# Kernel optimization log

Measured on AMD Instinct MI355X. Metric: run time of the kernel, lower is better.

The kernel has to match this reference:

```python
import jax, jax.numpy as jnp
import numpy as np
from jax import lax

G, BS = 8, 32  # group_num, blocksize


def conv(x, w, b=None, stride=1, pad=0):
    out = lax.conv_general_dilated(x, w, (stride, stride), [(pad, pad), (pad, pad)],
                                   dimension_numbers=('NCHW', 'OIHW', 'NCHW'))
    if b is not None:
        out = out + b[None, :, None, None]
    return out


def prelu(x, a):
    return jnp.where(x >= 0, x, a * x)


def reshape_adap(x, bs):
    # faithful vectorized form of My_Reshape_Adap: channel c = co*bs*bs + p*bs + q
    # goes to output[b, co, i*bs+p, j*bs+q]
    B, C, h, w = x.shape
    co = C // (bs * bs)
    return x.reshape(B, co, bs, bs, h, w).transpose(0, 1, 4, 2, 5, 3).reshape(B, co, h * bs, w * bs)


def setup_inputs() -> dict:
    key = jax.random.key(0)
    ks = jax.random.split(key, 24)
    rn = lambda k, shp, s: (jax.random.normal(k, shp, dtype=jnp.float32) * s)
    inp = {
        'x': rn(ks[0], (1, 1, 256, 256), 1.0),
        'sample_w': rn(ks[1], (G, 13, 1, 32, 32), 0.03),
        'up_w': rn(ks[2], (G, 1024, 13, 1, 1), 0.2),
        'up_b': rn(ks[3], (G, 1024), 0.02),
        'h1_w': rn(ks[4], (G, 64, 1, 3, 3), 0.2),
        'h1_b': rn(ks[5], (G, 64), 0.02),
        'h1_a': jnp.full((G,), 0.25, jnp.float32),
        'fus_w': rn(ks[6], (G - 1, 64, 128, 3, 3), 0.03),
        'fus_b': rn(ks[7], (G - 1, 64), 0.02),
        'fus_a': jnp.full((G - 1,), 0.25, jnp.float32),
        't2_w': rn(ks[8], (G, 64, 64, 3, 3), 0.04),
        't2_b': rn(ks[9], (G, 64), 0.02),
        't2_a': jnp.full((G,), 0.25, jnp.float32),
        't3_w': rn(ks[10], (G, 64, 64, 3, 3), 0.04),
        't3_b': rn(ks[11], (G, 64), 0.02),
        't3_a': jnp.full((G,), 0.25, jnp.float32),
        't4_w': rn(ks[12], (G, 64, 64, 3, 3), 0.04),
        't4_b': rn(ks[13], (G, 64), 0.02),
        't4_a': jnp.full((G,), 0.25, jnp.float32),
        't5_w': rn(ks[14], (G, 1, 64, 3, 3), 0.04),
        't5_b': rn(ks[15], (G, 1), 0.02),
    }
    return inp


def reference(x, sample_w, up_w, up_b, h1_w, h1_b, h1_a, fus_w, fus_b, fus_a,
              t2_w, t2_b, t2_a, t3_w, t3_b, t3_a, t4_w, t4_b, t4_a, t5_w, t5_b):
    outs = []
    feature = None
    for m in range(G):
        # SamplingModule: conv(1->13, k=32, s=32, no bias)
        s = conv(x, sample_w[m], stride=BS)
        # HeadBlock: 1x1 upsample (13->1024) + block scatter reshape + conv(1->64)+PReLU
        u = conv(s, up_w[m], up_b[m])
        r = reshape_adap(u, BS)                       # [B,1,H,W]
        h = prelu(conv(r, h1_w[m], h1_b[m], pad=1), h1_a[m])  # [B,64,H,W]
        if m == 0:
            feature = h
        else:
            # Fusion_concate: conv(128->64)+PReLU on channel concat
            cat = jnp.concatenate([feature, h], axis=1)
            feature = prelu(conv(cat, fus_w[m - 1], fus_b[m - 1], pad=1), fus_a[m - 1])
        t = prelu(conv(feature, t2_w[m], t2_b[m], pad=1), t2_a[m])
        t = prelu(conv(t, t3_w[m], t3_b[m], pad=1), t3_a[m])
        t = prelu(conv(t, t4_w[m], t4_b[m], pad=1), t4_a[m])
        outs.append(conv(t, t5_w[m], t5_b[m], pad=1))
    return jnp.stack(outs)  # [G, B, 1, H, W]
```

## Files before the change

### kernel.cpp

```cpp
#include <hip/hip_runtime.h>

constexpr int H = 256, W = 256, NPIX = H * W;
constexpr int PW = 258;
constexpr size_t PLANE = (size_t)PW * PW * 64;

typedef _Float16 half8 __attribute__((ext_vector_type(8)));
typedef _Float16 half4 __attribute__((ext_vector_type(4)));
typedef float    f32x4 __attribute__((ext_vector_type(4)));
typedef float    f32x16 __attribute__((ext_vector_type(16)));

__device__ __forceinline__ void gl16(const _Float16* g, _Float16* l)
{
    __builtin_amdgcn_global_load_lds(
        (const __attribute__((address_space(1))) unsigned int*)g,
        (__attribute__((address_space(3))) unsigned int*)l, 16, 0, 0);
}

__global__ __launch_bounds__(256)
void prep_k(const float* __restrict__ x, const float* __restrict__ sw,
            const float* __restrict__ uw, const float* __restrict__ ub,
            const float* __restrict__ t2w, const float* __restrict__ t3w,
            const float* __restrict__ t4w, const float* __restrict__ fusw,
            _Float16* __restrict__ planes, _Float16* __restrict__ w16,
            float* __restrict__ r_all)
{
    const int b = blockIdx.x, t = threadIdx.x;
    for (int idx = b * 256 + t; idx < 24 * 1028 * 8; idx += 512 * 256) {
        int c = idx & 7, rem = idx >> 3;
        int p = rem / 1028, bb = rem % 1028;
        int gy, gx;
        if (bb < 258)      { gy = 0;            gx = bb; }
        else if (bb < 516) { gy = 257;          gx = bb - 258; }
        else if (bb < 772) { gy = bb - 516 + 1; gx = 0; }
        else               { gy = bb - 772 + 1; gx = 257; }
        f32x4 z = {0.f, 0.f, 0.f, 0.f};
        *(f32x4*)(planes + (size_t)p * PLANE + ((size_t)(gy * PW + gx) * 64) + c * 8) = z;
    }
    for (int idx = b * 256 + t; idx < 38 * 36864; idx += 512 * 256) {
        int blk = idx / 36864, r2 = idx % 36864;
        int e = r2 & 7, co = (r2 >> 3) & 63, hh = (r2 >> 9) & 1, kk = (r2 >> 10) & 3,
            tap = r2 >> 12;
        const float* src; int cin, cib;
        if (blk < 24) {
            int which = blk >> 3, m = blk & 7;
            src = (which == 0 ? t2w : which == 1 ? t3w : t4w) + (size_t)m * 64 * 64 * 9;
            cin = 64; cib = 0;
        } else {
            int f = (blk - 24) >> 1; cib = ((blk - 24) & 1) * 64;
            src = fusw + (size_t)f * 64 * 128 * 9; cin = 128;
        }
        int ci = cib + (kk * 2 + hh) * 8 + e;
        w16[idx] = (_Float16)src[((size_t)co * cin + ci) * 9 + tap];
    }
    {
        int m = b >> 6, ij = b & 63;
        int i = ij >> 3, j = ij & 7;
        __shared__ float s_lds[16];
        if (t < 208) {
            int c = t >> 4, sub = t & 15;
            float acc = 0.f;
            for (int k = sub * 64; k < sub * 64 + 64; ++k) {
                int p = k >> 5, q = k & 31;
                acc += x[(i * 32 + p) * W + (j * 32 + q)] * sw[(m * 13 + c) * 1024 + k];
            }
            #pragma unroll
            for (int off = 8; off; off >>= 1) acc += __shfl_down(acc, off, 16);
            if (sub == 0) s_lds[c] = acc;
        }
        __syncthreads();
        const float* uwm = uw + m * 1024 * 13;
        float* rm = r_all + m * NPIX;
        #pragma unroll
        for (int pi = 0; pi < 4; ++pi) {
            int px = pi * 256 + t;
            int p = px >> 5, q = px & 31;
            int oc = p * 32 + q;
            float acc = ub[m * 1024 + oc];
            #pragma unroll
            for (int c = 0; c < 13; ++c) acc = fmaf(uwm[oc * 13 + c], s_lds[c], acc);
            rm[((i * 32 + p) << 8) + j * 32 + q] = acc;
        }
    }
}

__global__ __launch_bounds__(256)
void h1_k(const float* __restrict__ r_all, const float* __restrict__ w,
          const float* __restrict__ b, const float* __restrict__ a,
          _Float16* __restrict__ f0)
{
    const float* r = r_all;
    const int t = threadIdx.x;
    const int px = t & 63, cog = t >> 6;
    const int y = blockIdx.x >> 2;
    const int x = ((blockIdx.x & 3) << 6) + px;
    float v[9];
    #pragma unroll
    for (int dy = 0; dy < 3; ++dy) {
        int gy = y + dy - 1;
        #pragma unroll
        for (int dx = 0; dx < 3; ++dx) {
            int gx = x + dx - 1;
            v[dy*3+dx] = ((unsigned)gy < 256u && (unsigned)gx < 256u)
                       ? r[(gy << 8) + gx] : 0.f;
        }
    }
    const float slope = a[0];
    _Float16* op = f0 + ((size_t)((y + 1) * PW + (x + 1))) * 64 + cog * 16;
    #pragma unroll
    for (int cg2 = 0; cg2 < 2; ++cg2) {
        half8 o;
        #pragma unroll
        for (int j = 0; j < 8; ++j) {
            int co = cog * 16 + cg2 * 8 + j;
            float acc = b[co];
            #pragma unroll
            for (int k = 0; k < 9; ++k) acc = fmaf(v[k], w[co*9+k], acc);
            acc = acc >= 0.f ? acc : slope * acc;
            o[j] = (_Float16)acc;
        }
        *(half8*)(op + cg2 * 8) = o;
    }
}

__global__ __launch_bounds__(128, 2)
void conv_mfma_k(const _Float16* __restrict__ in0, const _Float16* __restrict__ w0,
                 const float* __restrict__ bias, const float* __restrict__ alpha,
                 _Float16* __restrict__ out)
{
    const int t    = threadIdx.x;
    const int lane = t & 63;
    const int wv   = t >> 6;
    const int b    = blockIdx.x;
    const int m    = b >> 7;
    const int rem  = b & 127;
    const int xq   = rem & 3;
    const int y0   = (rem >> 2) << 3;
    const int x0   = xq << 6;

    const _Float16* inp0 = in0 + (size_t)m * PLANE;
    _Float16*       outp = out + (size_t)m * PLANE;
    const _Float16* wp0  = w0 + (size_t)m * 36864;
    const float*    bp   = bias + m * 64;
    const float     slope = alpha[m];

    const int h = lane >> 5, cl = lane & 31;
    const int cobase = wv * 32;

    extern __shared__ __align__(16) char smem[];
    _Float16* li = (_Float16*)smem;

    half8 Areg[36];
    #pragma unroll
    for (int tap = 0; tap < 9; ++tap)
        #pragma unroll
        for (int kk = 0; kk < 4; ++kk)
            Areg[tap*4+kk] = *(const half8*)(wp0 +
                (size_t)(((tap*4+kk)*2 + h)*64 + cobase + cl) * 8);

    auto stage_row = [&](int pr) {
        const int slot = pr & 3;
        #pragma unroll
        for (int i = 0; i < 5; ++i) {
            int f = i * 128 + t;
            if (i < 4 || f < 528) {
                int hx = f >> 3, c = f & 7;
                gl16(inp0 + ((size_t)(pr * PW + x0 + hx) * 64 + (c ^ (hx & 7)) * 8),
                     li + (size_t)(slot * 528 + f) * 8);
            }
        }
    };

    f32x16 acc0, acc1;

    stage_row(y0); stage_row(y0 + 1); stage_row(y0 + 2);
    __syncthreads();
    #pragma unroll 1
    for (int s = 0; s < 8; ++s) {
        if (s < 7) stage_row(y0 + s + 3);
        #pragma unroll
        for (int q = 0; q < 4; ++q)
            #pragma unroll
            for (int j = 0; j < 4; ++j) {
                float bb = bp[cobase + q * 8 + 4 * h + j];
                acc0[q*4+j] = bb; acc1[q*4+j] = bb;
            }
        __builtin_amdgcn_s_setprio(1);
        #pragma unroll
        for (int tap = 0; tap < 9; ++tap) {
            const int dy = tap / 3, dx = tap % 3;
            const int slot = (y0 + s + dy) & 3;
            const int hx0 = cl + dx;
            const int hx1 = hx0 + 32;
            const int sw8 = hx0 & 7;
            #pragma unroll
            for (int kk = 0; kk < 4; ++kk) {
                const int c = kk * 2 + h;
                half8 b0 = *(const half8*)(li + ((size_t)(slot*528 + hx0*8 + (c ^ sw8))) * 8);
                half8 b1 = *(const half8*)(li + ((size_t)(slot*528 + hx1*8 + (c ^ sw8))) * 8);
                acc0 = __builtin_amdgcn_mfma_f32_32x32x16_f16(Areg[tap*4+kk], b0, acc0, 0, 0, 0);
                acc1 = __builtin_amdgcn_mfma_f32_32x32x16_f16(Areg[tap*4+kk], b1, acc1, 0, 0, 0);
            }
        }
        __builtin_amdgcn_s_setprio(0);
        const int y = y0 + s;
        #pragma unroll
        for (int pt = 0; pt < 2; ++pt) {
            const size_t gp = (size_t)((y + 1) * PW + (x0 + pt * 32 + cl + 1)) * 64;
            const f32x16& A0 = pt ? acc1 : acc0;
            #pragma unroll
            for (int q = 0; q < 4; ++q) {
                half4 v0;
                #pragma unroll
                for (int j = 0; j < 4; ++j) {
                    float xv = A0[q*4+j];
                    xv = xv >= 0.f ? xv : slope * xv;
                    v0[j] = (_Float16)v0[j];
                    v0[j] = (_Float16)xv;
                }
                *(half4*)(outp + gp + cobase + q * 8 + 4 * h) = v0;
            }
        }
        if (s < 7) {
            asm volatile("s_waitcnt vmcnt(8)" ::: "memory");
            __builtin_amdgcn_s_barrier();
            __builtin_amdgcn_sched_barrier(0);
        }
    }
}

__global__ __launch_bounds__(256, 2)
void fus_k(const _Float16* __restrict__ fprev, const float* __restrict__ rm,
           const float* __restrict__ h1w, const float* __restrict__ h1b,
           const float* __restrict__ h1a,
           const _Float16* __restrict__ wf, const _Float16* __restrict__ wh,
           const float* __restrict__ bias, const float* __restrict__ alpha,
           _Float16* __restrict__ outp)
{
    const int t = threadIdx.x, lane = t & 63, wv = t >> 6;
    const int b = blockIdx.x;
    const int xcd = b & 7, u = b >> 3, xq = u & 3, band = u >> 2;
    const int y0 = xcd * 32 + band * 2, x0 = xq * 64;
    const int h = lane >> 5, cl = lane & 31;
    const int px0 = (wv & 1) * 32, cobase = (wv >> 1) * 32;

    __shared__ __align__(16) _Float16 ringF[4 * 528 * 8];
    __shared__ __align__(16) _Float16 ringH[4 * 528 * 8];

    #pragma unroll
    for (int i = 0; i < 9; ++i) {
        int idx = i * 256 + t;
        if (i < 8 || idx < 2112) {
            int r = idx / 528, f = idx - r * 528;
            int hx = f >> 3, c = f & 7;
            gl16(fprev + ((size_t)((y0 + r) * PW + x0 + hx) * 64 + (c ^ (hx & 7)) * 8),
                 ringF + (size_t)idx * 8);
        }
    }
    {
        const int c8 = t & 7;
        float wreg[72];
        #pragma unroll
        for (int i = 0; i < 18; ++i)
            *(f32x4*)(wreg + i * 4) = *(const f32x4*)(h1w + c8 * 72 + i * 4);
        float b8[8];
        #pragma unroll
        for (int j = 0; j < 8; ++j) b8[j] = h1b[c8 * 8 + j];
        const float hs = h1a[0];

        #pragma unroll
        for (int it = 0; it < 9; ++it) {
            int idx = it * 256 + t;
            if (it < 8 || idx < 2112) {
                int pl = idx >> 3;
                int r  = pl / 66, hx = pl - r * 66;
                int gy = y0 - 1 + r, gx = x0 - 1 + hx;
                half8 o = {0,0,0,0,0,0,0,0};
                if ((unsigned)gy < 256u && (unsigned)gx < 256u) {
                    float v[9];
                    #pragma unroll
                    for (int dy = 0; dy < 3; ++dy) {
                        int ry = gy + dy - 1;
                        #pragma unroll
                        for (int dx = 0; dx < 3; ++dx) {
                            int rx = gx + dx - 1;
                            v[dy*3+dx] = ((unsigned)ry < 256u && (unsigned)rx < 256u)
                                       ? rm[(ry << 8) + rx] : 0.f;
                        }
                    }
                    #pragma unroll
                    for (int j = 0; j < 8; ++j) {
                        float av = b8[j];
                        #pragma unroll
                        for (int k = 0; k < 9; ++k) av = fmaf(v[k], wreg[j*9+k], av);
                        av = av >= 0.f ? av : hs * av;
                        o[j] = (_Float16)av;
                    }
                }
                *(half8*)(ringH + (size_t)(r * 528 + hx * 8 + (c8 ^ (hx & 7))) * 8) = o;
            }
        }
    }
    __builtin_amdgcn_sched_barrier(0);

    half8 Areg[36];
    auto load_A = [&](const _Float16* w) {
        #pragma unroll
        for (int tap = 0; tap < 9; ++tap)
            #pragma unroll
            for (int kk = 0; kk < 4; ++kk)
                Areg[tap*4+kk] = *(const half8*)(w +
                    (size_t)(((tap*4+kk)*2 + h)*64 + cobase + cl) * 8);
    };
    load_A(wf);

    f32x16 acc0, acc1;
    #pragma unroll
    for (int q = 0; q < 4; ++q)
        #pragma unroll
        for (int j = 0; j < 4; ++j) {
            float bb = bias[cobase + q * 8 + 4 * h + j];
            acc0[q*4+j] = bb; acc1[q*4+j] = bb;
        }

    __syncthreads();

    auto cpass = [&](const _Float16* ring) {
        __builtin_amdgcn_s_setprio(1);
        #pragma unroll
        for (int tap = 0; tap < 9; ++tap) {
            const int dy = tap / 3, dx = tap % 3;
            const int hx = px0 + cl + dx;
            const int sw = hx & 7;
            #pragma unroll
            for (int kk = 0; kk < 4; ++kk) {
                const int c = kk * 2 + h;
                half8 b0 = *(const half8*)(ring + ((size_t)(((dy    )*528) + hx*8 + (c ^ sw))) * 8);
                half8 b1 = *(const half8*)(ring + ((size_t)(((dy + 1)*528) + hx*8 + (c ^ sw))) * 8);
                acc0 = __builtin_amdgcn_mfma_f32_32x32x16_f16(Areg[tap*4+kk], b0, acc0, 0, 0, 0);
                acc1 = __builtin_amdgcn_mfma_f32_32x32x16_f16(Areg[tap*4+kk], b1, acc1, 0, 0, 0);
            }
        }
        __builtin_amdgcn_s_setprio(0);
    };

    cpass(ringF);
    load_A(wh);
    cpass(ringH);

    const float slope = alpha[0];
    #pragma unroll
    for (int s = 0; s < 2; ++s) {
        const size_t gp = (size_t)((y0 + s + 1) * PW + (x0 + px0 + cl + 1)) * 64 + cobase;
        const f32x16& A0 = s ? acc1 : acc0;
        #pragma unroll
        for (int q = 0; q < 4; ++q) {
            half4 v;
            #pragma unroll
            for (int j = 0; j < 4; ++j) {
                float xv = A0[q*4+j];
                xv = xv >= 0.f ? xv : slope * xv;
                v[j] = (_Float16)xv;
            }
            *(half4*)(outp + gp + q * 8 + 4 * h) = v;
        }
    }
}

__global__ __launch_bounds__(256, 2)
void t5_k(const _Float16* __restrict__ in_all, const float* __restrict__ w_all,
          const float* __restrict__ b_all, float* __restrict__ out_all)
{
    const int m = blockIdx.y;
    const _Float16* in = in_all + (size_t)m * PLANE;
    const float* w = w_all + m * 576;
    float* outp = out_all + m * NPIX;

    const int t = threadIdx.x;
    const int b = blockIdx.x;
    const int xcd = b & 7, u = b >> 3;
    const int xh = u & 1, band = u >> 1;
    const int y0 = xcd * 32 + band * 8;
    const int x0 = xh << 7;

    __shared__ __align__(16) _Float16 ring[4 * 130 * 64];
    __shared__ float wl[576];
    __shared__ float part[128];

    auto stage_row = [&](int pr) {
        const int slot = pr & 3;
        #pragma unroll
        for (int i = 0; i < 5; ++i) {
            int f = i * 256 + t;
            if (i < 4 || f < 1040) {
                int hx = f >> 3, c = f & 7;
                gl16(in + ((size_t)(pr * PW + x0 + hx) * 64 + (c ^ (hx & 7)) * 8),
                     ring + (size_t)(slot * 1040 + f) * 8);
            }
        }
    };

    stage_row(y0); stage_row(y0 + 1); stage_row(y0 + 2);
    #pragma unroll
    for (int i = 0; i < 3; ++i) { int idx = i*256 + t; if (idx < 576) wl[idx] = w[idx]; }
    __syncthreads();

    const int p = t & 127, chalf = t >> 7;
    #pragma unroll 1
    for (int s = 0; s < 8; ++s) {
        if (s < 7) stage_row(y0 + s + 3);
        float acc = 0.f;
        #pragma unroll
        for (int dy = 0; dy < 3; ++dy) {
            const int slot = (y0 + s + dy) & 3;
            #pragma unroll
            for (int dx = 0; dx < 3; ++dx) {
                const int hx = p + dx, sw = hx & 7, tap = dy * 3 + dx;
                #pragma unroll
                for (int kc = 0; kc < 4; ++kc) {
                    const int c8 = chalf * 4 + kc;
                    half8 vv = *(const half8*)(ring +
                        ((size_t)((slot*130 + hx)*8 + (c8 ^ sw))) * 8);
                    #pragma unroll
                    for (int e = 0; e < 8; ++e)
                        acc = fmaf((float)vv[e], wl[(c8 * 8 + e) * 9 + tap], acc);
                }
            }
        }
        if (chalf) part[p] = acc;
        __syncthreads();
        if (!chalf) outp[((y0 + s) << 8) + x0 + p] = part[p] + acc + b_all[m];
        __syncthreads();
    }
}

extern "C" void kernel_launch(void* const* d_in, const int* in_sizes, int n_in,
                              void* d_out, int out_size, void* d_ws, size_t ws_size,
                              hipStream_t stream)
{
    const float* x        = (const float*)d_in[0];
    const float* sample_w = (const float*)d_in[1];
    const float* up_w     = (const float*)d_in[2];
    const float* up_b     = (const float*)d_in[3];
    const float* h1_w     = (const float*)d_in[4];
    const float* h1_b     = (const float*)d_in[5];
    const float* h1_a     = (const float*)d_in[6];
    const float* fus_w    = (const float*)d_in[7];
    const float* fus_b    = (const float*)d_in[8];
    const float* fus_a    = (const float*)d_in[9];
    const float* t2_w     = (const float*)d_in[10];
    const float* t2_b     = (const float*)d_in[11];
    const float* t2_a     = (const float*)d_in[12];
    const float* t3_w     = (const float*)d_in[13];
    const float* t3_b     = (const float*)d_in[14];
    const float* t3_a     = (const float*)d_in[15];
    const float* t4_w     = (const float*)d_in[16];
    const float* t4_b     = (const float*)d_in[17];
    const float* t4_a     = (const float*)d_in[18];
    const float* t5_w     = (const float*)d_in[19];
    const float* t5_b     = (const float*)d_in[20];

    float* out = (float*)d_out;
    char*  wsb = (char*)d_ws;

    _Float16* w16    = (_Float16*)wsb;
    float*    r_all  = (float*)(wsb + 2801664);
    _Float16* f_all  = (_Float16*)(wsb + 4898816);
    _Float16* sc_all = f_all + 8 * PLANE;
    _Float16* t1_all = sc_all + 8 * PLANE;

    auto wblk = [&](int b) { return w16 + (size_t)b * 36864; };

    prep_k<<<512, 256, 0, stream>>>(x, sample_w, up_w, up_b,
                                    t2_w, t3_w, t4_w, fus_w,
                                    f_all, w16, r_all);
    h1_k<<<1024, 256, 0, stream>>>(r_all, h1_w, h1_b, h1_a, f_all);

    for (int m = 1; m < 8; ++m) {
        fus_k<<<512, 256, 0, stream>>>(
            f_all + (size_t)(m - 1) * PLANE,
            r_all + m * NPIX, h1_w + m * 576, h1_b + m * 64, h1_a + m,
            wblk(24 + (m - 1) * 2), wblk(24 + (m - 1) * 2 + 1),
            fus_b + (m - 1) * 64, fus_a + (m - 1),
            f_all + (size_t)m * PLANE);
    }

    const size_t LDSB = 33792;
    conv_mfma_k<<<1024, 128, LDSB, stream>>>(f_all, wblk(0), t2_b, t2_a, t1_all);
    conv_mfma_k<<<1024, 128, LDSB, stream>>>(t1_all, wblk(8), t3_b, t3_a, sc_all);
    conv_mfma_k<<<1024, 128, LDSB, stream>>>(sc_all, wblk(16), t4_b, t4_a, t1_all);
    t5_k<<<dim3(64, 8), 256, 0, stream>>>(t1_all, t5_w, t5_b, out);
}
```

Before: 393.2 us.

## Retile tail convs so each wave computes all 64 output channels over wider strips

The three 64->64 tail convolutions are re-tiled so each block covers a 128-pixel-wide strip with 8 rows, and each wave computes all 64 output channels for 64 pixels using four MFMA accumulators instead of 32 channels. Each B fragment read from LDS now feeds two MFMAs, which cuts LDS read traffic per MFMA and halves the number of blocks. The cost is twice the weight registers (72 half8) and twice the LDS per block (66560 bytes), with launch bounds dropped to one block per CU-slot. Occupancy falls and register pressure may cause spills.

```diff
diff --git a/kernel.cpp b/kernel.cpp
--- a/kernel.cpp
+++ b/kernel.cpp
@@ -122,7 +122,7 @@
     }
 }
 
-__global__ __launch_bounds__(128, 2)
+__global__ __launch_bounds__(128, 1)
 void conv_mfma_k(const _Float16* __restrict__ in0, const _Float16* __restrict__ w0,
                  const float* __restrict__ bias, const float* __restrict__ alpha,
                  _Float16* __restrict__ out)
@@ -131,11 +131,11 @@
     const int lane = t & 63;
     const int wv   = t >> 6;
     const int b    = blockIdx.x;
-    const int m    = b >> 7;
-    const int rem  = b & 127;
-    const int xq   = rem & 3;
-    const int y0   = (rem >> 2) << 3;
-    const int x0   = xq << 6;
+    const int m    = b >> 6;
+    const int rem  = b & 63;
+    const int xh   = rem & 1;
+    const int y0   = (rem >> 1) << 3;
+    const int x0   = xh << 7;
 
     const _Float16* inp0 = in0 + (size_t)m * PLANE;
     _Float16*       outp = out + (size_t)m * PLANE;
@@ -144,33 +144,36 @@
     const float     slope = alpha[m];
 
     const int h = lane >> 5, cl = lane & 31;
-    const int cobase = wv * 32;
+    const int px0 = wv << 6;
 
     extern __shared__ __align__(16) char smem[];
     _Float16* li = (_Float16*)smem;
 
-    half8 Areg[36];
+    half8 Areg0[36], Areg1[36];
     #pragma unroll
     for (int tap = 0; tap < 9; ++tap)
         #pragma unroll
-        for (int kk = 0; kk < 4; ++kk)
-            Areg[tap*4+kk] = *(const half8*)(wp0 +
-                (size_t)(((tap*4+kk)*2 + h)*64 + cobase + cl) * 8);
+        for (int kk = 0; kk < 4; ++kk) {
+            Areg0[tap*4+kk] = *(const half8*)(wp0 +
+                (size_t)(((tap*4+kk)*2 + h)*64 + cl) * 8);
+            Areg1[tap*4+kk] = *(const half8*)(wp0 +
+                (size_t)(((tap*4+kk)*2 + h)*64 + 32 + cl) * 8);
+        }
 
     auto stage_row = [&](int pr) {
         const int slot = pr & 3;
         #pragma unroll
-        for (int i = 0; i < 5; ++i) {
+        for (int i = 0; i < 9; ++i) {
             int f = i * 128 + t;
-            if (i < 4 || f < 528) {
+            if (i < 8 || f < 1040) {
                 int hx = f >> 3, c = f & 7;
                 gl16(inp0 + ((size_t)(pr * PW + x0 + hx) * 64 + (c ^ (hx & 7)) * 8),
-                     li + (size_t)(slot * 528 + f) * 8);
+                     li + (size_t)(slot * 1040 + f) * 8);
             }
         }
     };
 
-    f32x16 acc0, acc1;
+    f32x16 acc00, acc01, acc10, acc11;
 
     stage_row(y0); stage_row(y0 + 1); stage_row(y0 + 2);
     __syncthreads();
@@ -181,47 +184,51 @@
         for (int q = 0; q < 4; ++q)
             #pragma unroll
             for (int j = 0; j < 4; ++j) {
-                float bb = bp[cobase + q * 8 + 4 * h + j];
-                acc0[q*4+j] = bb; acc1[q*4+j] = bb;
+                float b0 = bp[q * 8 + 4 * h + j];
+                float b1 = bp[32 + q * 8 + 4 * h + j];
+                acc00[q*4+j] = b0; acc01[q*4+j] = b0;
+                acc10[q*4+j] = b1; acc11[q*4+j] = b1;
             }
         __builtin_amdgcn_s_setprio(1);
         #pragma unroll
         for (int tap = 0; tap < 9; ++tap) {
             const int dy = tap / 3, dx = tap % 3;
             const int slot = (y0 + s + dy) & 3;
-            const int hx0 = cl + dx;
+            const int hx0 = px0 + cl + dx;
             const int hx1 = hx0 + 32;
             const int sw8 = hx0 & 7;
             #pragma unroll
             for (int kk = 0; kk < 4; ++kk) {
                 const int c = kk * 2 + h;
-                half8 b0 = *(const half8*)(li + ((size_t)(slot*528 + hx0*8 + (c ^ sw8))) * 8);
-                half8 b1 = *(const half8*)(li + ((size_t)(slot*528 + hx1*8 + (c ^ sw8))) * 8);
-                acc0 = __builtin_amdgcn_mfma_f32_32x32x16_f16(Areg[tap*4+kk], b0, acc0, 0, 0, 0);
-                acc1 = __builtin_amdgcn_mfma_f32_32x32x16_f16(Areg[tap*4+kk], b1, acc1, 0, 0, 0);
+                half8 b0 = *(const half8*)(li + ((size_t)(slot*1040 + hx0*8 + (c ^ sw8))) * 8);
+                half8 b1 = *(const half8*)(li + ((size_t)(slot*1040 + hx1*8 + (c ^ sw8))) * 8);
+                acc00 = __builtin_amdgcn_mfma_f32_32x32x16_f16(Areg0[tap*4+kk], b0, acc00, 0, 0, 0);
+                acc01 = __builtin_amdgcn_mfma_f32_32x32x16_f16(Areg0[tap*4+kk], b1, acc01, 0, 0, 0);
+                acc10 = __builtin_amdgcn_mfma_f32_32x32x16_f16(Areg1[tap*4+kk], b0, acc10, 0, 0, 0);
+                acc11 = __builtin_amdgcn_mfma_f32_32x32x16_f16(Areg1[tap*4+kk], b1, acc11, 0, 0, 0);
             }
         }
         __builtin_amdgcn_s_setprio(0);
         const int y = y0 + s;
         #pragma unroll
         for (int pt = 0; pt < 2; ++pt) {
-            const size_t gp = (size_t)((y + 1) * PW + (x0 + pt * 32 + cl + 1)) * 64;
-            const f32x16& A0 = pt ? acc1 : acc0;
+            const size_t gp = (size_t)((y + 1) * PW + (x0 + px0 + pt * 32 + cl + 1)) * 64;
+            const f32x16& A0 = pt ? acc01 : acc00;
+            const f32x16& A1 = pt ? acc11 : acc10;
             #pragma unroll
             for (int q = 0; q < 4; ++q) {
-                half4 v0;
+                half4 v0, v1;
                 #pragma unroll
                 for (int j = 0; j < 4; ++j) {
-                    float xv = A0[q*4+j];
-                    xv = xv >= 0.f ? xv : slope * xv;
-                    v0[j] = (_Float16)v0[j];
-                    v0[j] = (_Float16)xv;
+                    float xv = A0[q*4+j]; xv = xv >= 0.f ? xv : slope * xv; v0[j] = (_Float16)xv;
+                    float yv = A1[q*4+j]; yv = yv >= 0.f ? yv : slope * yv; v1[j] = (_Float16)yv;
                 }
-                *(half4*)(outp + gp + cobase + q * 8 + 4 * h) = v0;
+                *(half4*)(outp + gp + q * 8 + 4 * h)      = v0;
+                *(half4*)(outp + gp + 32 + q * 8 + 4 * h) = v1;
             }
         }
         if (s < 7) {
-            asm volatile("s_waitcnt vmcnt(8)" ::: "memory");
+            asm volatile("s_waitcnt vmcnt(16)" ::: "memory");
             __builtin_amdgcn_s_barrier();
             __builtin_amdgcn_sched_barrier(0);
         }
@@ -484,9 +491,9 @@
             f_all + (size_t)m * PLANE);
     }
 
-    const size_t LDSB = 33792;
-    conv_mfma_k<<<1024, 128, LDSB, stream>>>(f_all, wblk(0), t2_b, t2_a, t1_all);
-    conv_mfma_k<<<1024, 128, LDSB, stream>>>(t1_all, wblk(8), t3_b, t3_a, sc_all);
-    conv_mfma_k<<<1024, 128, LDSB, stream>>>(sc_all, wblk(16), t4_b, t4_a, t1_all);
+    const size_t LDSB = 66560;
+    conv_mfma_k<<<512, 128, LDSB, stream>>>(f_all, wblk(0), t2_b, t2_a, t1_all);
+    conv_mfma_k<<<512, 128, LDSB, stream>>>(t1_all, wblk(8), t3_b, t3_a, sc_all);
+    conv_mfma_k<<<512, 128, LDSB, stream>>>(sc_all, wblk(16), t4_b, t4_a, t1_all);
     t5_k<<<dim3(64, 8), 256, 0, stream>>>(t1_all, t5_w, t5_b, out);
 }
```

Result: no change. 399.0 us (+1.5%).

## Fuse t4 conv with final t5 conv and widen conv_mfma tiles to 128 pixels

Applied to the files above, without the earlier changes.

Fuses the t4 64->64 MFMA conv with the 64->1 t5 conv. The t4 output rows are kept in an LDS ring and t5 is computed from them directly, with halo columns shared between neighbouring tiles via atomicAdd onto an output that prep_k pre-fills with the t5 bias. This removes one full 64-channel fp16 plane write and read-back per group. Separately, conv_mfma_k now uses 256 threads covering 128 pixels per block, doubling LDS to 66560 bytes, so each staged row is shared across more pixels. The costs are one recomputed halo row above and below each band, atomics at tile edges, and possibly lower occupancy from the larger LDS footprint.

```diff
diff --git a/kernel.cpp b/kernel.cpp
--- a/kernel.cpp
+++ b/kernel.cpp
@@ -21,8 +21,9 @@
             const float* __restrict__ uw, const float* __restrict__ ub,
             const float* __restrict__ t2w, const float* __restrict__ t3w,
             const float* __restrict__ t4w, const float* __restrict__ fusw,
+            const float* __restrict__ t5b,
             _Float16* __restrict__ planes, _Float16* __restrict__ w16,
-            float* __restrict__ r_all)
+            float* __restrict__ r_all, float* __restrict__ out)
 {
     const int b = blockIdx.x, t = threadIdx.x;
     for (int idx = b * 256 + t; idx < 24 * 1028 * 8; idx += 512 * 256) {
@@ -52,6 +53,8 @@
         int ci = cib + (kk * 2 + hh) * 8 + e;
         w16[idx] = (_Float16)src[((size_t)co * cin + ci) * 9 + tap];
     }
+    for (int idx = b * 256 + t; idx < 8 * NPIX; idx += 512 * 256)
+        out[idx] = t5b[idx >> 16];
     {
         int m = b >> 6, ij = b & 63;
         int i = ij >> 3, j = ij & 7;
@@ -122,7 +125,7 @@
     }
 }
 
-__global__ __launch_bounds__(128, 2)
+__global__ __launch_bounds__(256, 2)
 void conv_mfma_k(const _Float16* __restrict__ in0, const _Float16* __restrict__ w0,
                  const float* __restrict__ bias, const float* __restrict__ alpha,
                  _Float16* __restrict__ out)
@@ -131,20 +134,20 @@
     const int lane = t & 63;
     const int wv   = t >> 6;
     const int b    = blockIdx.x;
-    const int m    = b >> 7;
-    const int rem  = b & 127;
-    const int xq   = rem & 3;
-    const int y0   = (rem >> 2) << 3;
-    const int x0   = xq << 6;
+    const int m    = b >> 6;
+    const int rem  = b & 63;
+    const int xh   = rem & 1;
+    const int y0   = (rem >> 1) << 3;
 
     const _Float16* inp0 = in0 + (size_t)m * PLANE;
     _Float16*       outp = out + (size_t)m * PLANE;
     const _Float16* wp0  = w0 + (size_t)m * 36864;
     const float*    bp   = bias + m * 64;
     const float     slope = alpha[m];
+    const int x0 = xh << 7;
 
     const int h = lane >> 5, cl = lane & 31;
-    const int cobase = wv * 32;
+    const int px0 = (wv & 1) * 64, cobase = (wv >> 1) * 32;
 
     extern __shared__ __align__(16) char smem[];
     _Float16* li = (_Float16*)smem;
@@ -161,11 +164,11 @@
         const int slot = pr & 3;
         #pragma unroll
         for (int i = 0; i < 5; ++i) {
-            int f = i * 128 + t;
-            if (i < 4 || f < 528) {
+            int f = i * 256 + t;
+            if (i < 4 || f < 1040) {
                 int hx = f >> 3, c = f & 7;
                 gl16(inp0 + ((size_t)(pr * PW + x0 + hx) * 64 + (c ^ (hx & 7)) * 8),
-                     li + (size_t)(slot * 528 + f) * 8);
+                     li + (size_t)(slot * 1040 + f) * 8);
             }
         }
     };
@@ -189,14 +192,14 @@
         for (int tap = 0; tap < 9; ++tap) {
             const int dy = tap / 3, dx = tap % 3;
             const int slot = (y0 + s + dy) & 3;
-            const int hx0 = cl + dx;
+            const int hx0 = px0 + cl + dx;
             const int hx1 = hx0 + 32;
             const int sw8 = hx0 & 7;
             #pragma unroll
             for (int kk = 0; kk < 4; ++kk) {
                 const int c = kk * 2 + h;
-                half8 b0 = *(const half8*)(li + ((size_t)(slot*528 + hx0*8 + (c ^ sw8))) * 8);
-                half8 b1 = *(const half8*)(li + ((size_t)(slot*528 + hx1*8 + (c ^ sw8))) * 8);
+                half8 b0 = *(const half8*)(li + ((size_t)((slot*130 + hx0)*8 + (c ^ sw8))) * 8);
+                half8 b1 = *(const half8*)(li + ((size_t)((slot*130 + hx1)*8 + (c ^ sw8))) * 8);
                 acc0 = __builtin_amdgcn_mfma_f32_32x32x16_f16(Areg[tap*4+kk], b0, acc0, 0, 0, 0);
                 acc1 = __builtin_amdgcn_mfma_f32_32x32x16_f16(Areg[tap*4+kk], b1, acc1, 0, 0, 0);
             }
@@ -205,7 +208,7 @@
         const int y = y0 + s;
         #pragma unroll
         for (int pt = 0; pt < 2; ++pt) {
-            const size_t gp = (size_t)((y + 1) * PW + (x0 + pt * 32 + cl + 1)) * 64;
+            const size_t gp = (size_t)((y + 1) * PW + (x0 + px0 + pt * 32 + cl + 1)) * 64;
             const f32x16& A0 = pt ? acc1 : acc0;
             #pragma unroll
             for (int q = 0; q < 4; ++q) {
@@ -214,7 +217,6 @@
                 for (int j = 0; j < 4; ++j) {
                     float xv = A0[q*4+j];
                     xv = xv >= 0.f ? xv : slope * xv;
-                    v0[j] = (_Float16)v0[j];
                     v0[j] = (_Float16)xv;
                 }
                 *(half4*)(outp + gp + cobase + q * 8 + 4 * h) = v0;
@@ -367,69 +369,177 @@
 }
 
 __global__ __launch_bounds__(256, 2)
-void t5_k(const _Float16* __restrict__ in_all, const float* __restrict__ w_all,
-          const float* __restrict__ b_all, float* __restrict__ out_all)
+void t45_k(const _Float16* __restrict__ in_all, const _Float16* __restrict__ w4_all,
+           const float* __restrict__ b4, const float* __restrict__ a4,
+           const float* __restrict__ w5_all, const float* __restrict__ b5,
+           float* __restrict__ out_all)
 {
-    const int m = blockIdx.y;
+    const int t = threadIdx.x, lane = t & 63, wv = t >> 6;
+    const int b = blockIdx.x;
+    const int m = b >> 7, u = b & 127, xq = u & 3, band = u >> 2;
+    const int x0 = xq << 6, y0 = band << 3;
+
     const _Float16* in = in_all + (size_t)m * PLANE;
-    const float* w = w_all + m * 576;
-    float* outp = out_all + m * NPIX;
-
-    const int t = threadIdx.x;
-    const int b = blockIdx.x;
-    const int xcd = b & 7, u = b >> 3;
-    const int xh = u & 1, band = u >> 1;
-    const int y0 = xcd * 32 + band * 8;
-    const int x0 = xh << 7;
-
-    __shared__ __align__(16) _Float16 ring[4 * 130 * 64];
+    const _Float16* wp = w4_all + (size_t)m * 36864;
+    const float*    bp = b4 + m * 64;
+    const float  slope = a4[m];
+    const float*    w5 = w5_all + m * 576;
+    const float  bias5 = b5[m];
+    float*        outp = out_all + m * NPIX;
+
+    const int h = lane >> 5, cl = lane & 31;
+    const int px0 = (wv & 1) * 32, coh = wv >> 1, cobase = coh * 32;
+
+    __shared__ __align__(16) _Float16 inring[4 * 528 * 8];
+    __shared__ __align__(16) _Float16 t4ring[4 * 512 * 8];
     __shared__ float wl[576];
-    __shared__ float part[128];
-
-    auto stage_row = [&](int pr) {
-        const int slot = pr & 3;
-        #pragma unroll
-        for (int i = 0; i < 5; ++i) {
+    __shared__ float part[4][66];
+
+    #pragma unroll
+    for (int i = 0; i < 3; ++i) { int idx = i*256 + t; if (idx < 576) wl[idx] = w5[idx]; }
+
+    half8 Areg[36];
+    #pragma unroll
+    for (int tap = 0; tap < 9; ++tap)
+        #pragma unroll
+        for (int kk = 0; kk < 4; ++kk)
+            Areg[tap*4+kk] = *(const half8*)(wp +
+                (size_t)(((tap*4+kk)*2 + h)*64 + cobase + cl) * 8);
+
+    auto stage_row = [&](int r) {
+        if (r < -1 || r > 256) return;
+        const int slot = (r + 4) & 3;
+        #pragma unroll
+        for (int i = 0; i < 3; ++i) {
             int f = i * 256 + t;
-            if (i < 4 || f < 1040) {
+            if (f < 528) {
                 int hx = f >> 3, c = f & 7;
-                gl16(in + ((size_t)(pr * PW + x0 + hx) * 64 + (c ^ (hx & 7)) * 8),
-                     ring + (size_t)(slot * 1040 + f) * 8);
+                gl16(in + ((size_t)((r + 1) * PW + x0 + hx) * 64 + (c ^ (hx & 7)) * 8),
+                     inring + (size_t)(slot * 528 + f) * 8);
             }
         }
     };
 
-    stage_row(y0); stage_row(y0 + 1); stage_row(y0 + 2);
-    #pragma unroll
-    for (int i = 0; i < 3; ++i) { int idx = i*256 + t; if (idx < 576) wl[idx] = w[idx]; }
+    stage_row(y0 - 2); stage_row(y0 - 1); stage_row(y0);
     __syncthreads();
 
-    const int p = t & 127, chalf = t >> 7;
     #pragma unroll 1
-    for (int s = 0; s < 8; ++s) {
-        if (s < 7) stage_row(y0 + s + 3);
-        float acc = 0.f;
-        #pragma unroll
-        for (int dy = 0; dy < 3; ++dy) {
-            const int slot = (y0 + s + dy) & 3;
-            #pragma unroll
-            for (int dx = 0; dx < 3; ++dx) {
-                const int hx = p + dx, sw = hx & 7, tap = dy * 3 + dx;
+    for (int s = 0; s < 10; ++s) {
+        const int r = y0 - 1 + s;
+        stage_row(r + 2);
+
+        const int slot4 = (r + 4) & 3;
+        const int px = px0 + cl;
+        if (r >= 0 && r <= 255) {
+            f32x16 acc;
+            #pragma unroll
+            for (int q = 0; q < 4; ++q)
                 #pragma unroll
-                for (int kc = 0; kc < 4; ++kc) {
-                    const int c8 = chalf * 4 + kc;
-                    half8 vv = *(const half8*)(ring +
-                        ((size_t)((slot*130 + hx)*8 + (c8 ^ sw))) * 8);
+                for (int j = 0; j < 4; ++j)
+                    acc[q*4+j] = bp[cobase + q * 8 + 4 * h + j];
+            __builtin_amdgcn_s_setprio(1);
+            #pragma unroll
+            for (int tap = 0; tap < 9; ++tap) {
+                const int dy = tap / 3, dx = tap % 3;
+                const int sl = (r - 1 + dy + 4) & 3;
+                const int hx = px0 + cl + dx;
+                const int sw = hx & 7;
+                #pragma unroll
+                for (int kk = 0; kk < 4; ++kk) {
+                    const int c = kk * 2 + h;
+                    half8 bb = *(const half8*)(inring +
+                        ((size_t)(sl*528 + hx*8 + (c ^ sw))) * 8);
+                    acc = __builtin_amdgcn_mfma_f32_32x32x16_f16(Areg[tap*4+kk], bb, acc, 0, 0, 0);
+                }
+            }
+            __builtin_amdgcn_s_setprio(0);
+            #pragma unroll
+            for (int q = 0; q < 4; ++q) {
+                half4 v;
+                #pragma unroll
+                for (int j = 0; j < 4; ++j) {
+                    float xv = acc[q*4+j];
+                    xv = xv >= 0.f ? xv : slope * xv;
+                    v[j] = (_Float16)xv;
+                }
+                int cq = coh * 4 + q;
+                *(half4*)(t4ring + (size_t)(slot4*512 + px*8 + (cq ^ (px & 7))) * 8 + h * 4) = v;
+            }
+        } else {
+            half4 z = {0, 0, 0, 0};
+            #pragma unroll
+            for (int q = 0; q < 4; ++q) {
+                int cq = coh * 4 + q;
+                *(half4*)(t4ring + (size_t)(slot4*512 + px*8 + (cq ^ (px & 7))) * 8 + h * 4) = z;
+            }
+        }
+
+        asm volatile("s_waitcnt lgkmcnt(0)" ::: "memory");
+        __builtin_amdgcn_s_barrier();
+        __builtin_amdgcn_sched_barrier(0);
+
+        if (s >= 2) {
+            const int ro = r - 1;
+            const int p5 = t & 63, cg = t >> 6;
+            float own = 0.f, eL = 0.f, eR = 0.f;
+            #pragma unroll
+            for (int dy = 0; dy < 3; ++dy) {
+                const int sl = (ro - 1 + dy + 4) & 3;
+                #pragma unroll
+                for (int dx = 0; dx < 3; ++dx) {
+                    const int L = p5 + dx - 1;
+                    if (L >= 0 && L <= 63) {
+                        #pragma unroll
+                        for (int c2 = 0; c2 < 2; ++c2) {
+                            const int c8 = cg * 2 + c2;
+                            half8 v = *(const half8*)(t4ring +
+                                ((size_t)(sl*512 + L*8 + (c8 ^ (L & 7)))) * 8);
+                            #pragma unroll
+                            for (int e = 0; e < 8; ++e)
+                                own = fmaf((float)v[e], wl[(c8*8+e)*9 + dy*3 + dx], own);
+                        }
+                    }
+                }
+                if (p5 == 0) {
                     #pragma unroll
-                    for (int e = 0; e < 8; ++e)
-                        acc = fmaf((float)vv[e], wl[(c8 * 8 + e) * 9 + tap], acc);
+                    for (int c2 = 0; c2 < 2; ++c2) {
+                        const int c8 = cg * 2 + c2;
+                        half8 v = *(const half8*)(t4ring + ((size_t)(sl*512 + (c8 ^ 0))) * 8);
+                        #pragma unroll
+                        for (int e = 0; e < 8; ++e)
+                            eL = fmaf((float)v[e], wl[(c8*8+e)*9 + dy*3 + 2], eL);
+                    }
                 }
-            }
-        }
-        if (chalf) part[p] = acc;
-        __syncthreads();
-        if (!chalf) outp[((y0 + s) << 8) + x0 + p] = part[p] + acc + b_all[m];
-        __syncthreads();
+                if (p5 == 63) {
+                    #pragma unroll
+                    for (int c2 = 0; c2 < 2; ++c2) {
+                        const int c8 = cg * 2 + c2;
+                        half8 v = *(const half8*)(t4ring +
+                            ((size_t)(sl*512 + 63*8 + (c8 ^ 7))) * 8);
+                        #pragma unroll
+                        for (int e = 0; e < 8; ++e)
+                            eR = fmaf((float)v[e], wl[(c8*8+e)*9 + dy*3 + 0], eR);
+                    }
+                }
+            }
+            part[cg][p5 + 1] = own;
+            if (p5 == 0)  part[cg][0]  = eL;
+            if (p5 == 63) part[cg][65] = eR;
+        }
+
+        asm volatile("s_waitcnt vmcnt(0) lgkmcnt(0)" ::: "memory");
+        __builtin_amdgcn_s_barrier();
+        __builtin_amdgcn_sched_barrier(0);
+
+        if (s >= 2 && t < 66) {
+            const int ro = r - 1;
+            float sum = part[0][t] + part[1][t] + part[2][t] + part[3][t];
+            int gx = x0 + t - 1;
+            if (t >= 2 && t <= 63)
+                outp[(ro << 8) + gx] = sum + bias5;
+            else if (gx >= 0 && gx < 256)
+                atomicAdd(&outp[(ro << 8) + gx], sum);
+        }
     }
 }
 
@@ -471,8 +581,8 @@
     auto wblk = [&](int b) { return w16 + (size_t)b * 36864; };
 
     prep_k<<<512, 256, 0, stream>>>(x, sample_w, up_w, up_b,
-                                    t2_w, t3_w, t4_w, fus_w,
-                                    f_all, w16, r_all);
+                                    t2_w, t3_w, t4_w, fus_w, t5_b,
+                                    f_all, w16, r_all, out);
     h1_k<<<1024, 256, 0, stream>>>(r_all, h1_w, h1_b, h1_a, f_all);
 
     for (int m = 1; m < 8; ++m) {
@@ -484,9 +594,8 @@
             f_all + (size_t)m * PLANE);
     }
 
-    const size_t LDSB = 33792;
-    conv_mfma_k<<<1024, 128, LDSB, stream>>>(f_all, wblk(0), t2_b, t2_a, t1_all);
-    conv_mfma_k<<<1024, 128, LDSB, stream>>>(t1_all, wblk(8), t3_b, t3_a, sc_all);
-    conv_mfma_k<<<1024, 128, LDSB, stream>>>(sc_all, wblk(16), t4_b, t4_a, t1_all);
-    t5_k<<<dim3(64, 8), 256, 0, stream>>>(t1_all, t5_w, t5_b, out);
+    const size_t LDSB = 66560;
+    conv_mfma_k<<<512, 256, LDSB, stream>>>(f_all, wblk(0), t2_b, t2_a, t1_all);
+    conv_mfma_k<<<512, 256, LDSB, stream>>>(t1_all, wblk(8), t3_b, t3_a, sc_all);
+    t45_k<<<1024, 256, 0, stream>>>(sc_all, wblk(16), t4_b, t4_a, t5_w, t5_b, out);
 }
```

Result: slower. 410.1 us (+4.3%).

## Fuse h1 head conv into first fusion kernel and widen conv tiles

Applied to the files above, without the earlier changes.

Removes the standalone h1_k launch by computing the m=0 head features inside a templated first fusion kernel, which also writes them to the f0 plane for the later tail convs. The tail conv kernel now uses 256-thread blocks covering 128-pixel-wide strips, with four waves splitting pixels and output channels. Each staged halo row is shared by more pixels, which cuts redundant global loads and halves the block count. In exchange, LDS use per block doubles to about 65KB, which may reduce occupancy, and the first fusion kernel does extra scalar work to compute both head planes.

```diff
diff --git a/kernel.cpp b/kernel.cpp
--- a/kernel.cpp
+++ b/kernel.cpp
@@ -83,46 +83,7 @@
     }
 }
 
-__global__ __launch_bounds__(256)
-void h1_k(const float* __restrict__ r_all, const float* __restrict__ w,
-          const float* __restrict__ b, const float* __restrict__ a,
-          _Float16* __restrict__ f0)
-{
-    const float* r = r_all;
-    const int t = threadIdx.x;
-    const int px = t & 63, cog = t >> 6;
-    const int y = blockIdx.x >> 2;
-    const int x = ((blockIdx.x & 3) << 6) + px;
-    float v[9];
-    #pragma unroll
-    for (int dy = 0; dy < 3; ++dy) {
-        int gy = y + dy - 1;
-        #pragma unroll
-        for (int dx = 0; dx < 3; ++dx) {
-            int gx = x + dx - 1;
-            v[dy*3+dx] = ((unsigned)gy < 256u && (unsigned)gx < 256u)
-                       ? r[(gy << 8) + gx] : 0.f;
-        }
-    }
-    const float slope = a[0];
-    _Float16* op = f0 + ((size_t)((y + 1) * PW + (x + 1))) * 64 + cog * 16;
-    #pragma unroll
-    for (int cg2 = 0; cg2 < 2; ++cg2) {
-        half8 o;
-        #pragma unroll
-        for (int j = 0; j < 8; ++j) {
-            int co = cog * 16 + cg2 * 8 + j;
-            float acc = b[co];
-            #pragma unroll
-            for (int k = 0; k < 9; ++k) acc = fmaf(v[k], w[co*9+k], acc);
-            acc = acc >= 0.f ? acc : slope * acc;
-            o[j] = (_Float16)acc;
-        }
-        *(half8*)(op + cg2 * 8) = o;
-    }
-}
-
-__global__ __launch_bounds__(128, 2)
+__global__ __launch_bounds__(256, 2)
 void conv_mfma_k(const _Float16* __restrict__ in0, const _Float16* __restrict__ w0,
                  const float* __restrict__ bias, const float* __restrict__ alpha,
                  _Float16* __restrict__ out)
@@ -131,20 +92,20 @@
     const int lane = t & 63;
     const int wv   = t >> 6;
     const int b    = blockIdx.x;
-    const int m    = b >> 7;
-    const int rem  = b & 127;
-    const int xq   = rem & 3;
-    const int y0   = (rem >> 2) << 3;
-    const int x0   = xq << 6;
+    const int m    = b >> 6;
+    const int rem  = b & 63;
+    const int xh   = rem & 1;
+    const int y0   = (rem >> 1) << 3;
 
     const _Float16* inp0 = in0 + (size_t)m * PLANE;
     _Float16*       outp = out + (size_t)m * PLANE;
     const _Float16* wp0  = w0 + (size_t)m * 36864;
     const float*    bp   = bias + m * 64;
     const float     slope = alpha[m];
+    const int x0 = xh << 7;
 
     const int h = lane >> 5, cl = lane & 31;
-    const int cobase = wv * 32;
+    const int px0 = (wv & 1) * 64, cobase = (wv >> 1) * 32;
 
     extern __shared__ __align__(16) char smem[];
     _Float16* li = (_Float16*)smem;
@@ -161,11 +122,11 @@
         const int slot = pr & 3;
         #pragma unroll
         for (int i = 0; i < 5; ++i) {
-            int f = i * 128 + t;
-            if (i < 4 || f < 528) {
+            int f = i * 256 + t;
+            if (i < 4 || f < 1040) {
                 int hx = f >> 3, c = f & 7;
                 gl16(inp0 + ((size_t)(pr * PW + x0 + hx) * 64 + (c ^ (hx & 7)) * 8),
-                     li + (size_t)(slot * 528 + f) * 8);
+                     li + (size_t)(slot * 1040 + f) * 8);
             }
         }
     };
@@ -189,14 +150,14 @@
         for (int tap = 0; tap < 9; ++tap) {
             const int dy = tap / 3, dx = tap % 3;
             const int slot = (y0 + s + dy) & 3;
-            const int hx0 = cl + dx;
+            const int hx0 = px0 + cl + dx;
             const int hx1 = hx0 + 32;
             const int sw8 = hx0 & 7;
             #pragma unroll
             for (int kk = 0; kk < 4; ++kk) {
                 const int c = kk * 2 + h;
-                half8 b0 = *(const half8*)(li + ((size_t)(slot*528 + hx0*8 + (c ^ sw8))) * 8);
-                half8 b1 = *(const half8*)(li + ((size_t)(slot*528 + hx1*8 + (c ^ sw8))) * 8);
+                half8 b0 = *(const half8*)(li + ((size_t)((slot*130 + hx0)*8 + (c ^ sw8))) * 8);
+                half8 b1 = *(const half8*)(li + ((size_t)((slot*130 + hx1)*8 + (c ^ sw8))) * 8);
                 acc0 = __builtin_amdgcn_mfma_f32_32x32x16_f16(Areg[tap*4+kk], b0, acc0, 0, 0, 0);
                 acc1 = __builtin_amdgcn_mfma_f32_32x32x16_f16(Areg[tap*4+kk], b1, acc1, 0, 0, 0);
             }
@@ -205,7 +166,7 @@
         const int y = y0 + s;
         #pragma unroll
         for (int pt = 0; pt < 2; ++pt) {
-            const size_t gp = (size_t)((y + 1) * PW + (x0 + pt * 32 + cl + 1)) * 64;
+            const size_t gp = (size_t)((y + 1) * PW + (x0 + px0 + pt * 32 + cl + 1)) * 64;
             const f32x16& A0 = pt ? acc1 : acc0;
             #pragma unroll
             for (int q = 0; q < 4; ++q) {
@@ -214,7 +175,6 @@
                 for (int j = 0; j < 4; ++j) {
                     float xv = A0[q*4+j];
                     xv = xv >= 0.f ? xv : slope * xv;
-                    v0[j] = (_Float16)v0[j];
                     v0[j] = (_Float16)xv;
                 }
                 *(half4*)(outp + gp + cobase + q * 8 + 4 * h) = v0;
@@ -228,10 +188,14 @@
     }
 }
 
+template <int FIRST>
 __global__ __launch_bounds__(256, 2)
-void fus_k(const _Float16* __restrict__ fprev, const float* __restrict__ rm,
-           const float* __restrict__ h1w, const float* __restrict__ h1b,
-           const float* __restrict__ h1a,
+void fus_k(const _Float16* __restrict__ fprev, _Float16* __restrict__ f0out,
+           const float* __restrict__ rm_prev, const float* __restrict__ rm_cur,
+           const float* __restrict__ h1w_prev, const float* __restrict__ h1b_prev,
+           const float* __restrict__ h1a_prev,
+           const float* __restrict__ h1w_cur, const float* __restrict__ h1b_cur,
+           const float* __restrict__ h1a_cur,
            const _Float16* __restrict__ wf, const _Float16* __restrict__ wh,
            const float* __restrict__ bias, const float* __restrict__ alpha,
            _Float16* __restrict__ outp)
@@ -246,17 +210,8 @@
     __shared__ __align__(16) _Float16 ringF[4 * 528 * 8];
     __shared__ __align__(16) _Float16 ringH[4 * 528 * 8];
 
-    #pragma unroll
-    for (int i = 0; i < 9; ++i) {
-        int idx = i * 256 + t;
-        if (i < 8 || idx < 2112) {
-            int r = idx / 528, f = idx - r * 528;
-            int hx = f >> 3, c = f & 7;
-            gl16(fprev + ((size_t)((y0 + r) * PW + x0 + hx) * 64 + (c ^ (hx & 7)) * 8),
-                 ringF + (size_t)idx * 8);
-        }
-    }
-    {
+    auto hcomp = [&](const float* rm, const float* h1w, const float* h1b,
+                     float hs, _Float16* ring, _Float16* f0w) {
         const int c8 = t & 7;
         float wreg[72];
         #pragma unroll
@@ -265,7 +220,6 @@
         float b8[8];
         #pragma unroll
         for (int j = 0; j < 8; ++j) b8[j] = h1b[c8 * 8 + j];
-        const float hs = h1a[0];
 
         #pragma unroll
         for (int it = 0; it < 9; ++it) {
@@ -295,11 +249,30 @@
                         av = av >= 0.f ? av : hs * av;
                         o[j] = (_Float16)av;
                     }
+                    if (f0w && r >= 1 && r <= 2 && hx >= 1 && hx <= 64)
+                        *(half8*)(f0w + ((size_t)((gy + 1) * PW + (gx + 1)) * 64)
+                                  + c8 * 8) = o;
                 }
-                *(half8*)(ringH + (size_t)(r * 528 + hx * 8 + (c8 ^ (hx & 7))) * 8) = o;
-            }
-        }
-    }
+                *(half8*)(ring + (size_t)(r * 528 + hx * 8 + (c8 ^ (hx & 7))) * 8) = o;
+            }
+        }
+    };
+
+    if (FIRST) {
+        hcomp(rm_prev, h1w_prev, h1b_prev, h1a_prev[0], ringF, f0out);
+    } else {
+        #pragma unroll
+        for (int i = 0; i < 9; ++i) {
+            int idx = i * 256 + t;
+            if (i < 8 || idx < 2112) {
+                int r = idx / 528, f = idx - r * 528;
+                int hx = f >> 3, c = f & 7;
+                gl16(fprev + ((size_t)((y0 + r) * PW + x0 + hx) * 64 + (c ^ (hx & 7)) * 8),
+                     ringF + (size_t)idx * 8);
+            }
+        }
+    }
+    hcomp(rm_cur, h1w_cur, h1b_cur, h1a_cur[0], ringH, nullptr);
     __builtin_amdgcn_sched_barrier(0);
 
     half8 Areg[36];
@@ -473,20 +446,28 @@
     prep_k<<<512, 256, 0, stream>>>(x, sample_w, up_w, up_b,
                                     t2_w, t3_w, t4_w, fus_w,
                                     f_all, w16, r_all);
-    h1_k<<<1024, 256, 0, stream>>>(r_all, h1_w, h1_b, h1_a, f_all);
-
-    for (int m = 1; m < 8; ++m) {
-        fus_k<<<512, 256, 0, stream>>>(
-            f_all + (size_t)(m - 1) * PLANE,
-            r_all + m * NPIX, h1_w + m * 576, h1_b + m * 64, h1_a + m,
+
+    fus_k<1><<<512, 256, 0, stream>>>(
+        nullptr, f_all,
+        r_all, r_all + NPIX,
+        h1_w, h1_b, h1_a,
+        h1_w + 576, h1_b + 64, h1_a + 1,
+        wblk(24), wblk(25), fus_b, fus_a,
+        f_all + PLANE);
+    for (int m = 2; m < 8; ++m) {
+        fus_k<0><<<512, 256, 0, stream>>>(
+            f_all + (size_t)(m - 1) * PLANE, nullptr,
+            nullptr, r_all + m * NPIX,
+            nullptr, nullptr, nullptr,
+            h1_w + m * 576, h1_b + m * 64, h1_a + m,
             wblk(24 + (m - 1) * 2), wblk(24 + (m - 1) * 2 + 1),
             fus_b + (m - 1) * 64, fus_a + (m - 1),
             f_all + (size_t)m * PLANE);
     }
 
-    const size_t LDSB = 33792;
-    conv_mfma_k<<<1024, 128, LDSB, stream>>>(f_all, wblk(0), t2_b, t2_a, t1_all);
-    conv_mfma_k<<<1024, 128, LDSB, stream>>>(t1_all, wblk(8), t3_b, t3_a, sc_all);
-    conv_mfma_k<<<1024, 128, LDSB, stream>>>(sc_all, wblk(16), t4_b, t4_a, t1_all);
+    const size_t LDSB = 66560;
+    conv_mfma_k<<<512, 256, LDSB, stream>>>(f_all, wblk(0), t2_b, t2_a, t1_all);
+    conv_mfma_k<<<512, 256, LDSB, stream>>>(t1_all, wblk(8), t3_b, t3_a, sc_all);
+    conv_mfma_k<<<512, 256, LDSB, stream>>>(sc_all, wblk(16), t4_b, t4_a, t1_all);
     t5_k<<<dim3(64, 8), 256, 0, stream>>>(t1_all, t5_w, t5_b, out);
 }
```

After: 398.0 us. No clear change (+1.2%).
